# Kernel optimization log

Measured on AMD Instinct MI355X. Metric: run time of the kernel, lower is better.

Reference implementation:

```python
import jax, jax.numpy as jnp
import numpy as np
from jax import lax

B, CIN, H, W = 32, 256, 28, 28
COUT, KS, KEXP = 256, 3, 4
HIDDEN = int(CIN * 0.25)  # ratio hard-coded to 0.25 in the module


def setup_inputs() -> dict:
    key = jax.random.key(0)
    k1, k2, k3, k4 = jax.random.split(key, 4)
    x = jax.random.normal(k1, (B, CIN, H, W), dtype=jnp.float32)
    # SE (InvertedEx) params: fc1 (1x1 conv, no bias), fc2 (1x1 conv, bias)
    fc1_w = jax.random.normal(k2, (HIDDEN, CIN), dtype=jnp.float32) * np.float32(np.sqrt(2.0 / CIN))
    fc2_w = jax.random.normal(k3, (KEXP * COUT, HIDDEN), dtype=jnp.float32) * np.float32(np.sqrt(2.0 / HIDDEN))
    fc2_b = jnp.zeros((KEXP * COUT,), dtype=jnp.float32)
    # K expert conv kernels, he_std = sqrt(2) * (CIN*KS^2)^-0.5
    he_std = np.float32(np.sqrt(2.0) * (CIN * KS * KS) ** -0.5)
    weight = jax.random.normal(k4, (KEXP, COUT, CIN, KS, KS), dtype=jnp.float32) * he_std
    return {"x": x, "fc1_w": fc1_w, "fc2_w": fc2_w, "fc2_b": fc2_b, "weight": weight}


def reference(x, fc1_w, fc2_w, fc2_b, weight):
    # --- SE routing ---
    pooled = jnp.mean(x, axis=(2, 3))                        # [B, CIN]
    h = jax.nn.relu(pooled @ fc1_w.T)                        # [B, HIDDEN]
    y = (h @ fc2_w.T + fc2_b).reshape(B, KEXP, COUT)         # [B, K, COUT]
    prob = jax.nn.softmax(y / jnp.sqrt(jnp.float32(HIDDEN)), axis=1)  # softmax over K
    # --- aggregate per-sample kernels ---
    agg_w = jnp.einsum('bko,koihw->boihw', prob, weight)     # [B, COUT, CIN, KS, KS]
    # --- per-sample conv (batched implicit GEMM via vmap) ---
    def conv1(xi, wi):
        return lax.conv_general_dilated(
            xi[None], wi, window_strides=(1, 1), padding=((1, 1), (1, 1)),
            dimension_numbers=('NCHW', 'OIHW', 'NCHW'))[0]
    out = jax.vmap(conv1)(x, agg_w)                          # [B, COUT, H, W]
    return out
```

## Files before the change

kernel.cpp:

```cpp
#include <hip/hip_runtime.h>
#include <math.h>

#define B_    32
#define CIN_  256
#define HW_   784
#define H_    28
#define W_    28
#define COUT_ 256
#define KEXP_ 4
#define HID_  64

typedef short short8 __attribute__((ext_vector_type(8)));
typedef unsigned short ushort4v __attribute__((ext_vector_type(4)));
typedef float floatx16 __attribute__((ext_vector_type(16)));

__device__ __forceinline__ unsigned short f2bf(float f) {
    union { float f; unsigned int u; } v; v.f = f;
    unsigned int r = (v.u + 0x7FFFu + ((v.u >> 16) & 1u)) >> 16;
    return (unsigned short)r;
}

__global__ __launch_bounds__(256) void xpose_pool_kernel(const float* __restrict__ x,
                                                         unsigned short* __restrict__ x_t,
                                                         float* __restrict__ partial) {
    __shared__ float tile[32][33];
    int bid = blockIdx.x;
    int b   = bid / 200;
    int rem = bid - b * 200;
    int icg = rem / 25;
    int pxt = rem % 25;
    int ic0 = icg * 32;
    int px0 = pxt * 32;
    int t = threadIdx.x;
    int c = t & 31, rr = t >> 5;
    #pragma unroll
    for (int r = 0; r < 4; ++r) {
        int icr = rr + r * 8;
        int px = px0 + c;
        float v = (px < HW_) ? x[((size_t)(b * CIN_ + ic0 + icr)) * HW_ + px] : 0.f;
        tile[icr][c] = v;
    }
    __syncthreads();
    #pragma unroll
    for (int r = 0; r < 4; ++r) {
        int pxr = rr + r * 8;
        int px = px0 + pxr;
        if (px < HW_)
            x_t[((size_t)b * HW_ + px) * CIN_ + ic0 + c] = f2bf(tile[c][pxr]);
    }
    if (t < 32) {
        float s = 0.f;
        #pragma unroll
        for (int cc = 0; cc < 32; ++cc) s += tile[t][cc];
        partial[((size_t)b * 25 + pxt) * CIN_ + ic0 + t] = s * (1.0f / HW_);
    }
}

__global__ __launch_bounds__(256) void pool_kernel(const float* __restrict__ x,
                                                   float* __restrict__ pooled) {
    int w = blockIdx.x * 4 + (threadIdx.x >> 6);
    int lane = threadIdx.x & 63;
    const float* p = x + (size_t)w * HW_;
    float s = 0.f;
    for (int i = lane; i < HW_; i += 64) s += p[i];
    for (int off = 32; off; off >>= 1) s += __shfl_down(s, off);
    if (lane == 0) pooled[w] = s * (1.0f / HW_);
}

__global__ __launch_bounds__(256) void se3_kernel(const float* __restrict__ partial,
                                                  const float* __restrict__ fc1_w,
                                                  const float* __restrict__ fc2_w,
                                                  const float* __restrict__ fc2_b,
                                                  float* __restrict__ prob) {
    __shared__ float pl[CIN_];
    __shared__ float h[HID_];
    __shared__ float wb[16640];
    int b = blockIdx.x, t = threadIdx.x;
    {
        float s = 0.f;
        for (int pt = 0; pt < 25; ++pt)
            s += partial[((size_t)b * 25 + pt) * CIN_ + t];
        pl[t] = s;
    }
    #pragma unroll
    for (int i = 0; i < 16; ++i) {
        int l = t + i * 256;
        float4 v = *(const float4*)(fc1_w + (size_t)l * 4);
        int r = l >> 6, cc = (l & 63) * 4;
        float* dst = &wb[r * 257 + cc];
        dst[0] = v.x; dst[1] = v.y; dst[2] = v.z; dst[3] = v.w;
    }
    __syncthreads();
    if (t < HID_) {
        float s = 0.f;
        const float* wr = &wb[t * 257];
        for (int c = 0; c < CIN_; ++c) s += pl[c] * wr[c];
        h[t] = fmaxf(s, 0.f);
    }
    float yk[KEXP_];
    for (int k = 0; k < KEXP_; ++k) {
        __syncthreads();
        #pragma unroll
        for (int i = 0; i < 16; ++i) {
            int l = t + i * 256;
            float4 v = *(const float4*)(fc2_w + (size_t)k * COUT_ * HID_ + (size_t)l * 4);
            int o = l >> 4, jj = (l & 15) * 4;
            float* dst = &wb[o * 65 + jj];
            dst[0] = v.x; dst[1] = v.y; dst[2] = v.z; dst[3] = v.w;
        }
        __syncthreads();
        float s = fc2_b[k * COUT_ + t];
        const float* wr = &wb[t * 65];
        #pragma unroll
        for (int j = 0; j < HID_; ++j) s += h[j] * wr[j];
        yk[k] = s * 0.125f;
    }
    float m = yk[0];
    for (int k = 1; k < KEXP_; ++k) m = fmaxf(m, yk[k]);
    float e[KEXP_], sum = 0.f;
    for (int k = 0; k < KEXP_; ++k) { e[k] = expf(yk[k] - m); sum += e[k]; }
    float inv = 1.0f / sum;
    for (int k = 0; k < KEXP_; ++k)
        prob[b * (KEXP_ * COUT_) + k * COUT_ + t] = e[k] * inv;
}

__global__ __launch_bounds__(256) void se2_kernel(const float* __restrict__ pooled,
                                                  const float* __restrict__ fc1_w,
                                                  const float* __restrict__ fc2_w,
                                                  const float* __restrict__ fc2_b,
                                                  float* __restrict__ prob) {
    __shared__ float pl[CIN_];
    __shared__ float h[HID_];
    __shared__ float wb[16640];
    int b = blockIdx.x, t = threadIdx.x;
    pl[t] = pooled[b * CIN_ + t];
    #pragma unroll
    for (int i = 0; i < 16; ++i) {
        int l = t + i * 256;
        float4 v = *(const float4*)(fc1_w + (size_t)l * 4);
        int r = l >> 6, cc = (l & 63) * 4;
        float* dst = &wb[r * 257 + cc];
        dst[0] = v.x; dst[1] = v.y; dst[2] = v.z; dst[3] = v.w;
    }
    __syncthreads();
    if (t < HID_) {
        float s = 0.f;
        const float* wr = &wb[t * 257];
        for (int c = 0; c < CIN_; ++c) s += pl[c] * wr[c];
        h[t] = fmaxf(s, 0.f);
    }
    float yk[KEXP_];
    for (int k = 0; k < KEXP_; ++k) {
        __syncthreads();
        #pragma unroll
        for (int i = 0; i < 16; ++i) {
            int l = t + i * 256;
            float4 v = *(const float4*)(fc2_w + (size_t)k * COUT_ * HID_ + (size_t)l * 4);
            int o = l >> 4, jj = (l & 15) * 4;
            float* dst = &wb[o * 65 + jj];
            dst[0] = v.x; dst[1] = v.y; dst[2] = v.z; dst[3] = v.w;
        }
        __syncthreads();
        float s = fc2_b[k * COUT_ + t];
        const float* wr = &wb[t * 65];
        #pragma unroll
        for (int j = 0; j < HID_; ++j) s += h[j] * wr[j];
        yk[k] = s * 0.125f;
    }
    float m = yk[0];
    for (int k = 1; k < KEXP_; ++k) m = fmaxf(m, yk[k]);
    float e[KEXP_], sum = 0.f;
    for (int k = 0; k < KEXP_; ++k) { e[k] = expf(yk[k] - m); sum += e[k]; }
    float inv = 1.0f / sum;
    for (int k = 0; k < KEXP_; ++k)
        prob[b * (KEXP_ * COUT_) + k * COUT_ + t] = e[k] * inv;
}

__global__ __launch_bounds__(256) void agg4_kernel(const float* __restrict__ weight,
                                                   const float* __restrict__ prob,
                                                   unsigned short* __restrict__ agg) {
    __shared__ float ws_w[KEXP_ * CIN_ * 9];
    __shared__ float pb[KEXP_][16];
    int bid = blockIdx.x;
    int oc = bid & 255;
    int b0 = (bid >> 8) * 16;
    int t = threadIdx.x;
    #pragma unroll
    for (int i = 0; i < 9; ++i) {
        int e4 = t + i * 256;
        int k = e4 / 576;
        int r4 = e4 - k * 576;
        float4 v = *(const float4*)(weight + (size_t)k * 589824 + (size_t)oc * 2304 + (size_t)r4 * 4);
        *(float4*)&ws_w[e4 * 4] = v;
    }
    if (t < 64) {
        int k = t >> 4, bb = t & 15;
        pb[k][bb] = prob[(size_t)(b0 + bb) * (KEXP_ * COUT_) + k * COUT_ + oc];
    }
    __syncthreads();
    int icg = t & 63, blane = t >> 6;
    for (int rs = 0; rs < 9; ++rs) {
        float wv[4][4];
        #pragma unroll
        for (int q = 0; q < 4; ++q)
            #pragma unroll
            for (int k = 0; k < 4; ++k)
                wv[q][k] = ws_w[k * 2304 + (icg * 4 + q) * 9 + rs];
        #pragma unroll
        for (int bb = 0; bb < 4; ++bb) {
            int bidx = blane * 4 + bb;
            float p0 = pb[0][bidx], p1 = pb[1][bidx], p2 = pb[2][bidx], p3 = pb[3][bidx];
            ushort4v pack;
            #pragma unroll
            for (int q = 0; q < 4; ++q) {
                float s = p0 * wv[q][0] + p1 * wv[q][1] + p2 * wv[q][2] + p3 * wv[q][3];
                pack[q] = f2bf(s);
            }
            *(ushort4v*)(agg + (((size_t)(b0 + bidx) * 9 + rs) * COUT_ + oc) * CIN_ + icg * 4) = pack;
        }
    }
}

__global__ __launch_bounds__(256, 3) void conv_mfma4_kernel(const unsigned short* __restrict__ x_t,
                                                            const unsigned short* __restrict__ agg,
                                                            float* __restrict__ out) {
    __shared__ __align__(16) short Xs[6 * 35 * 72];

    int gid = blockIdx.x;
    int b      = gid & 31;
    int oc0    = ((gid >> 5) & 1) * 128;
    int rowblk = gid >> 6;
    int py0 = rowblk * 4;

    int t = threadIdx.x;
    int lane = t & 63, w = t >> 6;
    int ml = lane & 31, kh = lane >> 5;

    floatx16 acc[4];
    #pragma unroll
    for (int j = 0; j < 4; ++j)
        #pragma unroll
        for (int r = 0; r < 16; ++r) acc[j][r] = 0.f;

    const unsigned short* xtb = x_t + (size_t)b * HW_ * CIN_;
    const unsigned short* aln = agg + (((size_t)b * 9 * COUT_) + oc0 + w * 32 + ml) * CIN_ + kh * 8;

    short8 Acur0, Acur1, Acur2, Anext0, Anext1, Anext2;
    Acur0 = *(const short8*)(aln + (size_t)0 * (COUT_ * CIN_));
    Acur1 = *(const short8*)(aln + (size_t)3 * (COUT_ * CIN_));
    Acur2 = *(const short8*)(aln + (size_t)6 * (COUT_ * CIN_));
    int dxn = 1, kkn = 0, icn = 0;

    for (int c = 0; c < 4; ++c) {
        if (c) __syncthreads();
        #pragma unroll
        for (int i = 0; i < 7; ++i) {
            int l = t + i * 256;
            if (l < 1680) {
                int pos = l >> 3, g = l & 7;
                int row = pos / 35, col = pos - row * 35;
                int gy = py0 - 1 + row, gx = col - 1;
                short8 v = (short8)0;
                if ((unsigned)gy < 28u && (unsigned)gx < 28u)
                    v = *(const short8*)(xtb + ((size_t)(gy * W_ + gx)) * CIN_ + c * 64 + g * 8);
                *(short8*)&Xs[pos * 72 + g * 8] = v;
            }
        }
        __syncthreads();

        for (int kk = 0; kk < 4; ++kk) {
            for (int dx = 0; dx < 3; ++dx) {
                if (icn < 256) {
                    const unsigned short* ap = aln + icn + kkn * 16;
                    Anext0 = *(const short8*)(ap + (size_t)(0 * 3 + dxn) * (COUT_ * CIN_));
                    Anext1 = *(const short8*)(ap + (size_t)(1 * 3 + dxn) * (COUT_ * CIN_));
                    Anext2 = *(const short8*)(ap + (size_t)(2 * 3 + dxn) * (COUT_ * CIN_));
                    ++dxn;
                    if (dxn == 3) { dxn = 0; ++kkn; if (kkn == 4) { kkn = 0; icn += 64; } }
                }
                int va = (ml + dx) * 72 + kk * 16 + kh * 8;
                #pragma unroll
                for (int r = 0; r < 6; ++r) {
                    short8 Bf = *(const short8*)&Xs[r * 2520 + va];
                    if (r <= 3)
                        acc[r]     = __builtin_amdgcn_mfma_f32_32x32x16_bf16(Acur0, Bf, acc[r], 0, 0, 0);
                    if (r >= 1 && r <= 4)
                        acc[r - 1] = __builtin_amdgcn_mfma_f32_32x32x16_bf16(Acur1, Bf, acc[r - 1], 0, 0, 0);
                    if (r >= 2)
                        acc[r - 2] = __builtin_amdgcn_mfma_f32_32x32x16_bf16(Acur2, Bf, acc[r - 2], 0, 0, 0);
                }
                Acur0 = Anext0; Acur1 = Anext1; Acur2 = Anext2;
            }
        }
    }

    if (ml < W_) {
        #pragma unroll
        for (int j = 0; j < 4; ++j) {
            float* op = out + ((size_t)(b * COUT_ + oc0 + w * 32)) * HW_ + (py0 + j) * W_ + ml;
            #pragma unroll
            for (int r = 0; r < 16; ++r) {
                int ocd = (r & 3) + 8 * (r >> 2) + 4 * kh;
                op[(size_t)ocd * HW_] = acc[j][r];
            }
        }
    }
}

__global__ __launch_bounds__(256) void conv_kernel(const float* __restrict__ x,
                                                   const float* __restrict__ weight,
                                                   const float* __restrict__ prob,
                                                   float* __restrict__ out) {
    __shared__ float xs[30 * 30];
    __shared__ float wagg[8][32][12];
    __shared__ float pl[KEXP_][8];

    int b  = blockIdx.x >> 5;
    int o0 = (blockIdx.x & 31) * 8;
    int t  = threadIdx.x;

    if (t < 32) {
        int k = t >> 3, oc = t & 7;
        pl[k][oc] = prob[b * (KEXP_ * COUT_) + k * COUT_ + o0 + oc];
    }
    int p0 = t;
    int pr[4], pc[4];
    bool pv[4];
    #pragma unroll
    for (int j = 0; j < 4; ++j) {
        int p = p0 + j * 256;
        pv[j] = p < HW_;
        pr[j] = p / W_;
        pc[j] = p % W_;
    }
    float acc[8][4];
    #pragma unroll
    for (int oc = 0; oc < 8; ++oc)
        #pragma unroll
        for (int j = 0; j < 4; ++j) acc[oc][j] = 0.f;

    int aoc = t >> 5, aii = t & 31;

    for (int ic0 = 0; ic0 < CIN_; ic0 += 32) {
        __syncthreads();
        {
            float w9[9];
            #pragma unroll
            for (int j = 0; j < 9; ++j) w9[j] = 0.f;
            int i = ic0 + aii;
            #pragma unroll
            for (int k = 0; k < KEXP_; ++k) {
                float pk = pl[k][aoc];
                const float* wp = weight + ((size_t)(k * COUT_ + o0 + aoc) * CIN_ + i) * 9;
                #pragma unroll
                for (int j = 0; j < 9; ++j) w9[j] += pk * wp[j];
            }
            #pragma unroll
            for (int j = 0; j < 9; ++j) wagg[aoc][aii][j] = w9[j];
        }
        for (int ii = 0; ii < 32; ++ii) {
            int i = ic0 + ii;
            __syncthreads();
            const float* xp = x + (size_t)(b * CIN_ + i) * HW_;
            for (int e = t; e < 900; e += 256) {
                int ry = e / 30, cx = e - ry * 30;
                int gy = ry - 1, gx = cx - 1;
                float v = 0.f;
                if ((unsigned)gy < 28u && (unsigned)gx < 28u) v = xp[gy * W_ + gx];
                xs[e] = v;
            }
            __syncthreads();
            float xv[4][9];
            #pragma unroll
            for (int j = 0; j < 4; ++j) {
                if (pv[j]) {
                    const float* xr = &xs[pr[j] * 30 + pc[j]];
                    xv[j][0] = xr[0];  xv[j][1] = xr[1];  xv[j][2] = xr[2];
                    xv[j][3] = xr[30]; xv[j][4] = xr[31]; xv[j][5] = xr[32];
                    xv[j][6] = xr[60]; xv[j][7] = xr[61]; xv[j][8] = xr[62];
                } else {
                    #pragma unroll
                    for (int q = 0; q < 9; ++q) xv[j][q] = 0.f;
                }
            }
            #pragma unroll
            for (int oc = 0; oc < 8; ++oc) {
                float4 wa = *(const float4*)&wagg[oc][ii][0];
                float4 wb2 = *(const float4*)&wagg[oc][ii][4];
                float  wc = wagg[oc][ii][8];
                #pragma unroll
                for (int j = 0; j < 4; ++j) {
                    acc[oc][j] += xv[j][0] * wa.x + xv[j][1] * wa.y + xv[j][2] * wa.z
                                + xv[j][3] * wa.w + xv[j][4] * wb2.x + xv[j][5] * wb2.y
                                + xv[j][6] * wb2.z + xv[j][7] * wb2.w + xv[j][8] * wc;
                }
            }
        }
    }
    #pragma unroll
    for (int oc = 0; oc < 8; ++oc) {
        float* op = out + (size_t)(b * COUT_ + o0 + oc) * HW_ + p0;
        #pragma unroll
        for (int j = 0; j < 4; ++j)
            if (pv[j]) op[j * 256] = acc[oc][j];
    }
}

extern "C" void kernel_launch(void* const* d_in, const int* in_sizes, int n_in,
                              void* d_out, int out_size, void* d_ws, size_t ws_size,
                              hipStream_t stream) {
    const float* x     = (const float*)d_in[0];
    const float* fc1_w = (const float*)d_in[1];
    const float* fc2_w = (const float*)d_in[2];
    const float* fc2_b = (const float*)d_in[3];
    const float* weight= (const float*)d_in[4];
    float* out = (float*)d_out;

    char* ws = (char*)d_ws;
    float* prob = (float*)(ws);
    unsigned short* x_t = (unsigned short*)(ws + 131072);
    unsigned short* agg = (unsigned short*)(ws + 12976128);
    float* partial = (float*)(ws + 12976128);
    const size_t WS_NEED = 12976128 + (size_t)B_ * 9 * COUT_ * CIN_ * 2;

    if (ws_size >= WS_NEED) {
        xpose_pool_kernel<<<B_ * 8 * 25, 256, 0, stream>>>(x, x_t, partial);
        se3_kernel<<<B_, 256, 0, stream>>>(partial, fc1_w, fc2_w, fc2_b, prob);
        agg4_kernel<<<512, 256, 0, stream>>>(weight, prob, agg);
        conv_mfma4_kernel<<<448, 256, 0, stream>>>(x_t, agg, out);
    } else {
        float* pooled = (float*)(ws + 131072);
        pool_kernel<<<(B_ * CIN_) / 4, 256, 0, stream>>>(x, pooled);
        se2_kernel<<<B_, 256, 0, stream>>>(pooled, fc1_w, fc2_w, fc2_b, prob);
        conv_kernel<<<B_ * (COUT_ / 8), 256, 0, stream>>>(x, weight, prob, out);
    }
}
```

Measured before the change: 158.7 us.

## Fuse fc2+softmax into aggregation kernel and retile MFMA conv to 7-row blocks

The SE kernel is split so that one small kernel computes only the hidden layer. The fc2 projection and the softmax over experts move into the weight-aggregation kernel, which also relayouts the expert weights in shared memory so they can be read as float4 (ic-contiguous per tap). The conv kernel now covers 7 output rows per block with 64 output channels, and splits the waves into two row groups, with 512 blocks and launch bounds of 2. This aims to cut redundant X-tile loads from the 3-row halo and balance the grid, at the cost of more LDS per block and lower occupancy, with uneven work between the 4-row and 3-row wave groups.

```diff
diff --git a/kernel.cpp b/kernel.cpp
--- a/kernel.cpp
+++ b/kernel.cpp
@@ -56,25 +56,11 @@
     }
 }
 
-__global__ __launch_bounds__(256) void pool_kernel(const float* __restrict__ x,
-                                                   float* __restrict__ pooled) {
-    int w = blockIdx.x * 4 + (threadIdx.x >> 6);
-    int lane = threadIdx.x & 63;
-    const float* p = x + (size_t)w * HW_;
-    float s = 0.f;
-    for (int i = lane; i < HW_; i += 64) s += p[i];
-    for (int off = 32; off; off >>= 1) s += __shfl_down(s, off);
-    if (lane == 0) pooled[w] = s * (1.0f / HW_);
-}
-
-__global__ __launch_bounds__(256) void se3_kernel(const float* __restrict__ partial,
-                                                  const float* __restrict__ fc1_w,
-                                                  const float* __restrict__ fc2_w,
-                                                  const float* __restrict__ fc2_b,
-                                                  float* __restrict__ prob) {
+__global__ __launch_bounds__(256) void se_h_kernel(const float* __restrict__ partial,
+                                                   const float* __restrict__ fc1_w,
+                                                   float* __restrict__ h_g) {
     __shared__ float pl[CIN_];
-    __shared__ float h[HID_];
-    __shared__ float wb[16640];
+    __shared__ float wb[64 * 257];
     int b = blockIdx.x, t = threadIdx.x;
     {
         float s = 0.f;
@@ -95,146 +81,104 @@
         float s = 0.f;
         const float* wr = &wb[t * 257];
         for (int c = 0; c < CIN_; ++c) s += pl[c] * wr[c];
-        h[t] = fmaxf(s, 0.f);
-    }
-    float yk[KEXP_];
-    for (int k = 0; k < KEXP_; ++k) {
-        __syncthreads();
-        #pragma unroll
-        for (int i = 0; i < 16; ++i) {
-            int l = t + i * 256;
-            float4 v = *(const float4*)(fc2_w + (size_t)k * COUT_ * HID_ + (size_t)l * 4);
-            int o = l >> 4, jj = (l & 15) * 4;
-            float* dst = &wb[o * 65 + jj];
-            dst[0] = v.x; dst[1] = v.y; dst[2] = v.z; dst[3] = v.w;
-        }
-        __syncthreads();
-        float s = fc2_b[k * COUT_ + t];
-        const float* wr = &wb[t * 65];
-        #pragma unroll
-        for (int j = 0; j < HID_; ++j) s += h[j] * wr[j];
-        yk[k] = s * 0.125f;
-    }
-    float m = yk[0];
-    for (int k = 1; k < KEXP_; ++k) m = fmaxf(m, yk[k]);
-    float e[KEXP_], sum = 0.f;
-    for (int k = 0; k < KEXP_; ++k) { e[k] = expf(yk[k] - m); sum += e[k]; }
-    float inv = 1.0f / sum;
-    for (int k = 0; k < KEXP_; ++k)
-        prob[b * (KEXP_ * COUT_) + k * COUT_ + t] = e[k] * inv;
-}
-
-__global__ __launch_bounds__(256) void se2_kernel(const float* __restrict__ pooled,
-                                                  const float* __restrict__ fc1_w,
-                                                  const float* __restrict__ fc2_w,
-                                                  const float* __restrict__ fc2_b,
-                                                  float* __restrict__ prob) {
-    __shared__ float pl[CIN_];
-    __shared__ float h[HID_];
-    __shared__ float wb[16640];
-    int b = blockIdx.x, t = threadIdx.x;
-    pl[t] = pooled[b * CIN_ + t];
-    #pragma unroll
-    for (int i = 0; i < 16; ++i) {
-        int l = t + i * 256;
-        float4 v = *(const float4*)(fc1_w + (size_t)l * 4);
-        int r = l >> 6, cc = (l & 63) * 4;
-        float* dst = &wb[r * 257 + cc];
-        dst[0] = v.x; dst[1] = v.y; dst[2] = v.z; dst[3] = v.w;
-    }
-    __syncthreads();
-    if (t < HID_) {
-        float s = 0.f;
-        const float* wr = &wb[t * 257];
-        for (int c = 0; c < CIN_; ++c) s += pl[c] * wr[c];
-        h[t] = fmaxf(s, 0.f);
-    }
-    float yk[KEXP_];
-    for (int k = 0; k < KEXP_; ++k) {
-        __syncthreads();
-        #pragma unroll
-        for (int i = 0; i < 16; ++i) {
-            int l = t + i * 256;
-            float4 v = *(const float4*)(fc2_w + (size_t)k * COUT_ * HID_ + (size_t)l * 4);
-            int o = l >> 4, jj = (l & 15) * 4;
-            float* dst = &wb[o * 65 + jj];
-            dst[0] = v.x; dst[1] = v.y; dst[2] = v.z; dst[3] = v.w;
-        }
-        __syncthreads();
-        float s = fc2_b[k * COUT_ + t];
-        const float* wr = &wb[t * 65];
-        #pragma unroll
-        for (int j = 0; j < HID_; ++j) s += h[j] * wr[j];
-        yk[k] = s * 0.125f;
-    }
-    float m = yk[0];
-    for (int k = 1; k < KEXP_; ++k) m = fmaxf(m, yk[k]);
-    float e[KEXP_], sum = 0.f;
-    for (int k = 0; k < KEXP_; ++k) { e[k] = expf(yk[k] - m); sum += e[k]; }
-    float inv = 1.0f / sum;
-    for (int k = 0; k < KEXP_; ++k)
-        prob[b * (KEXP_ * COUT_) + k * COUT_ + t] = e[k] * inv;
-}
-
-__global__ __launch_bounds__(256) void agg4_kernel(const float* __restrict__ weight,
-                                                   const float* __restrict__ prob,
+        h_g[b * HID_ + t] = fmaxf(s, 0.f);
+    }
+}
+
+__global__ __launch_bounds__(256) void agg5_kernel(const float* __restrict__ weight,
+                                                   const float* __restrict__ h_g,
+                                                   const float* __restrict__ fc2_w,
+                                                   const float* __restrict__ fc2_b,
                                                    unsigned short* __restrict__ agg) {
     __shared__ float ws_w[KEXP_ * CIN_ * 9];
-    __shared__ float pb[KEXP_][16];
+    __shared__ float f2s[KEXP_ * HID_];
+    __shared__ float hb[16 * 65];
+    __shared__ float pb[KEXP_ * 16];
     int bid = blockIdx.x;
     int oc = bid & 255;
     int b0 = (bid >> 8) * 16;
     int t = threadIdx.x;
+
     #pragma unroll
     for (int i = 0; i < 9; ++i) {
         int e4 = t + i * 256;
         int k = e4 / 576;
         int r4 = e4 - k * 576;
         float4 v = *(const float4*)(weight + (size_t)k * 589824 + (size_t)oc * 2304 + (size_t)r4 * 4);
-        *(float4*)&ws_w[e4 * 4] = v;
-    }
+        int f = r4 * 4;
+        #pragma unroll
+        for (int q = 0; q < 4; ++q) {
+            int ic = (f + q) / 9, rs = (f + q) - ic * 9;
+            ws_w[k * 2304 + rs * 256 + ic] = ((const float*)&v)[q];
+        }
+    }
+    {
+        int k = t >> 6, j = t & 63;
+        f2s[t] = fc2_w[((size_t)(k * COUT_ + oc)) * HID_ + j];
+    }
+    #pragma unroll
+    for (int i = 0; i < 4; ++i) {
+        int l = t + i * 256;
+        if (l < 16 * HID_) {
+            int bq = l >> 6, j = l & 63;
+            hb[bq * 65 + j] = h_g[(size_t)(b0 + bq) * HID_ + j];
+        }
+    }
+    __syncthreads();
     if (t < 64) {
-        int k = t >> 4, bb = t & 15;
-        pb[k][bb] = prob[(size_t)(b0 + bb) * (KEXP_ * COUT_) + k * COUT_ + oc];
+        int bq = t >> 2, k = t & 3;
+        float s = fc2_b[k * COUT_ + oc];
+        const float* hr = &hb[bq * 65];
+        const float* fr = &f2s[k * HID_];
+        #pragma unroll
+        for (int j = 0; j < HID_; ++j) s += hr[j] * fr[j];
+        float y = s * 0.125f;
+        float m1 = fmaxf(y, __shfl_xor(y, 1));
+        float m  = fmaxf(m1, __shfl_xor(m1, 2));
+        float e = expf(y - m);
+        float s1 = e + __shfl_xor(e, 1);
+        float sm = s1 + __shfl_xor(s1, 2);
+        pb[k * 16 + bq] = e / sm;
     }
     __syncthreads();
+
     int icg = t & 63, blane = t >> 6;
     for (int rs = 0; rs < 9; ++rs) {
-        float wv[4][4];
-        #pragma unroll
-        for (int q = 0; q < 4; ++q)
-            #pragma unroll
-            for (int k = 0; k < 4; ++k)
-                wv[q][k] = ws_w[k * 2304 + (icg * 4 + q) * 9 + rs];
+        float4 w0 = *(const float4*)&ws_w[0 * 2304 + rs * 256 + icg * 4];
+        float4 w1 = *(const float4*)&ws_w[1 * 2304 + rs * 256 + icg * 4];
+        float4 w2 = *(const float4*)&ws_w[2 * 2304 + rs * 256 + icg * 4];
+        float4 w3 = *(const float4*)&ws_w[3 * 2304 + rs * 256 + icg * 4];
         #pragma unroll
         for (int bb = 0; bb < 4; ++bb) {
             int bidx = blane * 4 + bb;
-            float p0 = pb[0][bidx], p1 = pb[1][bidx], p2 = pb[2][bidx], p3 = pb[3][bidx];
+            float p0 = pb[0 * 16 + bidx], p1 = pb[1 * 16 + bidx];
+            float p2 = pb[2 * 16 + bidx], p3 = pb[3 * 16 + bidx];
             ushort4v pack;
-            #pragma unroll
-            for (int q = 0; q < 4; ++q) {
-                float s = p0 * wv[q][0] + p1 * wv[q][1] + p2 * wv[q][2] + p3 * wv[q][3];
-                pack[q] = f2bf(s);
-            }
+            pack[0] = f2bf(p0 * w0.x + p1 * w1.x + p2 * w2.x + p3 * w3.x);
+            pack[1] = f2bf(p0 * w0.y + p1 * w1.y + p2 * w2.y + p3 * w3.y);
+            pack[2] = f2bf(p0 * w0.z + p1 * w1.z + p2 * w2.z + p3 * w3.z);
+            pack[3] = f2bf(p0 * w0.w + p1 * w1.w + p2 * w2.w + p3 * w3.w);
             *(ushort4v*)(agg + (((size_t)(b0 + bidx) * 9 + rs) * COUT_ + oc) * CIN_ + icg * 4) = pack;
         }
     }
 }
 
-__global__ __launch_bounds__(256, 3) void conv_mfma4_kernel(const unsigned short* __restrict__ x_t,
+__global__ __launch_bounds__(256, 2) void conv_mfma5_kernel(const unsigned short* __restrict__ x_t,
                                                             const unsigned short* __restrict__ agg,
                                                             float* __restrict__ out) {
-    __shared__ __align__(16) short Xs[6 * 35 * 72];
+    __shared__ __align__(16) short Xs[9 * 35 * 72];
 
     int gid = blockIdx.x;
     int b      = gid & 31;
-    int oc0    = ((gid >> 5) & 1) * 128;
-    int rowblk = gid >> 6;
-    int py0 = rowblk * 4;
+    int ocq    = (gid >> 5) & 3;
+    int rowblk = gid >> 7;
+    int py0 = rowblk * 7;
 
     int t = threadIdx.x;
     int lane = t & 63, w = t >> 6;
+    int wo = w & 1, wr = w >> 1;
     int ml = lane & 31, kh = lane >> 5;
+    int oc0 = ocq * 64 + wo * 32;
 
     floatx16 acc[4];
     #pragma unroll
@@ -243,7 +187,7 @@
         for (int r = 0; r < 16; ++r) acc[j][r] = 0.f;
 
     const unsigned short* xtb = x_t + (size_t)b * HW_ * CIN_;
-    const unsigned short* aln = agg + (((size_t)b * 9 * COUT_) + oc0 + w * 32 + ml) * CIN_ + kh * 8;
+    const unsigned short* aln = agg + (((size_t)b * 9 * COUT_) + oc0 + ml) * CIN_ + kh * 8;
 
     short8 Acur0, Acur1, Acur2, Anext0, Anext1, Anext2;
     Acur0 = *(const short8*)(aln + (size_t)0 * (COUT_ * CIN_));
@@ -254,9 +198,9 @@
     for (int c = 0; c < 4; ++c) {
         if (c) __syncthreads();
         #pragma unroll
-        for (int i = 0; i < 7; ++i) {
+        for (int i = 0; i < 10; ++i) {
             int l = t + i * 256;
-            if (l < 1680) {
+            if (l < 2520) {
                 int pos = l >> 3, g = l & 7;
                 int row = pos / 35, col = pos - row * 35;
                 int gy = py0 - 1 + row, gx = col - 1;
@@ -279,25 +223,41 @@
                     if (dxn == 3) { dxn = 0; ++kkn; if (kkn == 4) { kkn = 0; icn += 64; } }
                 }
                 int va = (ml + dx) * 72 + kk * 16 + kh * 8;
-                #pragma unroll
-                for (int r = 0; r < 6; ++r) {
-                    short8 Bf = *(const short8*)&Xs[r * 2520 + va];
-                    if (r <= 3)
-                        acc[r]     = __builtin_amdgcn_mfma_f32_32x32x16_bf16(Acur0, Bf, acc[r], 0, 0, 0);
-                    if (r >= 1 && r <= 4)
-                        acc[r - 1] = __builtin_amdgcn_mfma_f32_32x32x16_bf16(Acur1, Bf, acc[r - 1], 0, 0, 0);
-                    if (r >= 2)
-                        acc[r - 2] = __builtin_amdgcn_mfma_f32_32x32x16_bf16(Acur2, Bf, acc[r - 2], 0, 0, 0);
+                if (wr == 0) {
+                    #pragma unroll
+                    for (int r = 0; r < 6; ++r) {
+                        short8 Bf = *(const short8*)&Xs[r * 2520 + va];
+                        if (r <= 3)
+                            acc[r]     = __builtin_amdgcn_mfma_f32_32x32x16_bf16(Acur0, Bf, acc[r], 0, 0, 0);
+                        if (r >= 1 && r <= 4)
+                            acc[r - 1] = __builtin_amdgcn_mfma_f32_32x32x16_bf16(Acur1, Bf, acc[r - 1], 0, 0, 0);
+                        if (r >= 2)
+                            acc[r - 2] = __builtin_amdgcn_mfma_f32_32x32x16_bf16(Acur2, Bf, acc[r - 2], 0, 0, 0);
+                    }
+                } else {
+                    #pragma unroll
+                    for (int rr2 = 0; rr2 < 5; ++rr2) {
+                        int r = rr2 + 4;
+                        short8 Bf = *(const short8*)&Xs[r * 2520 + va];
+                        int j0 = r - 4;
+                        if (j0 <= 2)
+                            acc[j0]     = __builtin_amdgcn_mfma_f32_32x32x16_bf16(Acur0, Bf, acc[j0], 0, 0, 0);
+                        if (r >= 5 && r - 5 <= 2)
+                            acc[r - 5]  = __builtin_amdgcn_mfma_f32_32x32x16_bf16(Acur1, Bf, acc[r - 5], 0, 0, 0);
+                        if (r >= 6)
+                            acc[r - 6]  = __builtin_amdgcn_mfma_f32_32x32x16_bf16(Acur2, Bf, acc[r - 6], 0, 0, 0);
+                    }
                 }
                 Acur0 = Anext0; Acur1 = Anext1; Acur2 = Anext2;
             }
         }
     }
 
+    int jbase = wr * 4;
+    int naccs = wr ? 3 : 4;
     if (ml < W_) {
-        #pragma unroll
-        for (int j = 0; j < 4; ++j) {
-            float* op = out + ((size_t)(b * COUT_ + oc0 + w * 32)) * HW_ + (py0 + j) * W_ + ml;
+        for (int j = 0; j < naccs; ++j) {
+            float* op = out + ((size_t)(b * COUT_ + oc0)) * HW_ + (py0 + jbase + j) * W_ + ml;
             #pragma unroll
             for (int r = 0; r < 16; ++r) {
                 int ocd = (r & 3) + 8 * (r >> 2) + 4 * kh;
@@ -305,6 +265,69 @@
             }
         }
     }
+}
+
+__global__ __launch_bounds__(256) void pool_kernel(const float* __restrict__ x,
+                                                   float* __restrict__ pooled) {
+    int w = blockIdx.x * 4 + (threadIdx.x >> 6);
+    int lane = threadIdx.x & 63;
+    const float* p = x + (size_t)w * HW_;
+    float s = 0.f;
+    for (int i = lane; i < HW_; i += 64) s += p[i];
+    for (int off = 32; off; off >>= 1) s += __shfl_down(s, off);
+    if (lane == 0) pooled[w] = s * (1.0f / HW_);
+}
+
+__global__ __launch_bounds__(256) void se2_kernel(const float* __restrict__ pooled,
+                                                  const float* __restrict__ fc1_w,
+                                                  const float* __restrict__ fc2_w,
+                                                  const float* __restrict__ fc2_b,
+                                                  float* __restrict__ prob) {
+    __shared__ float pl[CIN_];
+    __shared__ float h[HID_];
+    __shared__ float wb[16640];
+    int b = blockIdx.x, t = threadIdx.x;
+    pl[t] = pooled[b * CIN_ + t];
+    #pragma unroll
+    for (int i = 0; i < 16; ++i) {
+        int l = t + i * 256;
+        float4 v = *(const float4*)(fc1_w + (size_t)l * 4);
+        int r = l >> 6, cc = (l & 63) * 4;
+        float* dst = &wb[r * 257 + cc];
+        dst[0] = v.x; dst[1] = v.y; dst[2] = v.z; dst[3] = v.w;
+    }
+    __syncthreads();
+    if (t < HID_) {
+        float s = 0.f;
+        const float* wr = &wb[t * 257];
+        for (int c = 0; c < CIN_; ++c) s += pl[c] * wr[c];
+        h[t] = fmaxf(s, 0.f);
+    }
+    float yk[KEXP_];
+    for (int k = 0; k < KEXP_; ++k) {
+        __syncthreads();
+        #pragma unroll
+        for (int i = 0; i < 16; ++i) {
+            int l = t + i * 256;
+            float4 v = *(const float4*)(fc2_w + (size_t)k * COUT_ * HID_ + (size_t)l * 4);
+            int o = l >> 4, jj = (l & 15) * 4;
+            float* dst = &wb[o * 65 + jj];
+            dst[0] = v.x; dst[1] = v.y; dst[2] = v.z; dst[3] = v.w;
+        }
+        __syncthreads();
+        float s = fc2_b[k * COUT_ + t];
+        const float* wr = &wb[t * 65];
+        #pragma unroll
+        for (int j = 0; j < HID_; ++j) s += h[j] * wr[j];
+        yk[k] = s * 0.125f;
+    }
+    float m = yk[0];
+    for (int k = 1; k < KEXP_; ++k) m = fmaxf(m, yk[k]);
+    float e[KEXP_], sum = 0.f;
+    for (int k = 0; k < KEXP_; ++k) { e[k] = expf(yk[k] - m); sum += e[k]; }
+    float inv = 1.0f / sum;
+    for (int k = 0; k < KEXP_; ++k)
+        prob[b * (KEXP_ * COUT_) + k * COUT_ + t] = e[k] * inv;
 }
 
 __global__ __launch_bounds__(256) void conv_kernel(const float* __restrict__ x,
@@ -417,7 +440,7 @@
     float* out = (float*)d_out;
 
     char* ws = (char*)d_ws;
-    float* prob = (float*)(ws);
+    float* h_g  = (float*)(ws);
     unsigned short* x_t = (unsigned short*)(ws + 131072);
     unsigned short* agg = (unsigned short*)(ws + 12976128);
     float* partial = (float*)(ws + 12976128);
@@ -425,10 +448,11 @@
 
     if (ws_size >= WS_NEED) {
         xpose_pool_kernel<<<B_ * 8 * 25, 256, 0, stream>>>(x, x_t, partial);
-        se3_kernel<<<B_, 256, 0, stream>>>(partial, fc1_w, fc2_w, fc2_b, prob);
-        agg4_kernel<<<512, 256, 0, stream>>>(weight, prob, agg);
-        conv_mfma4_kernel<<<448, 256, 0, stream>>>(x_t, agg, out);
+        se_h_kernel<<<B_, 256, 0, stream>>>(partial, fc1_w, h_g);
+        agg5_kernel<<<512, 256, 0, stream>>>(weight, h_g, fc2_w, fc2_b, agg);
+        conv_mfma5_kernel<<<512, 256, 0, stream>>>(x_t, agg, out);
     } else {
+        float* prob = (float*)(ws);
         float* pooled = (float*)(ws + 131072);
         pool_kernel<<<(B_ * CIN_) / 4, 256, 0, stream>>>(x, pooled);
         se2_kernel<<<B_, 256, 0, stream>>>(pooled, fc1_w, fc2_w, fc2_b, prob);
```

Result: slower. 265.4 us (+67.2%).

## Fuse SE routing into aggregation kernel and widen transpose tile

Applied to the files above, without the earlier changes.

Removes the separate SE kernel: the transpose kernel now handles 64 channels per block with 16-byte bf16 stores and also writes a transposed fc1 weight. The aggregation kernel recomputes pooling, fc1, fc2 and softmax for its 16 samples, which takes one launch and one dependency off the critical path. The cost is redundant SE work in each of the 512 aggregation blocks. The conv kernel's grid and launch bounds change to 512 blocks with an added row guard.

```diff
diff --git a/kernel.cpp b/kernel.cpp
--- a/kernel.cpp
+++ b/kernel.cpp
@@ -20,171 +20,74 @@
     return (unsigned short)r;
 }
 
-__global__ __launch_bounds__(256) void xpose_pool_kernel(const float* __restrict__ x,
-                                                         unsigned short* __restrict__ x_t,
-                                                         float* __restrict__ partial) {
-    __shared__ float tile[32][33];
+__global__ __launch_bounds__(256) void xpose2_kernel(const float* __restrict__ x,
+                                                     const float* __restrict__ fc1_w,
+                                                     unsigned short* __restrict__ x_t,
+                                                     float* __restrict__ partial,
+                                                     float* __restrict__ fc1T) {
+    __shared__ float tile[64][33];
     int bid = blockIdx.x;
-    int b   = bid / 200;
-    int rem = bid - b * 200;
+    int b   = bid / 100;
+    int rem = bid - b * 100;
     int icg = rem / 25;
     int pxt = rem % 25;
-    int ic0 = icg * 32;
+    int ic0 = icg * 64;
     int px0 = pxt * 32;
     int t = threadIdx.x;
-    int c = t & 31, rr = t >> 5;
-    #pragma unroll
-    for (int r = 0; r < 4; ++r) {
-        int icr = rr + r * 8;
-        int px = px0 + c;
+    int pxl = t & 31, icr0 = t >> 5;
+    #pragma unroll
+    for (int r = 0; r < 8; ++r) {
+        int icr = icr0 + r * 8;
+        int px = px0 + pxl;
         float v = (px < HW_) ? x[((size_t)(b * CIN_ + ic0 + icr)) * HW_ + px] : 0.f;
-        tile[icr][c] = v;
+        tile[icr][pxl] = v;
     }
     __syncthreads();
-    #pragma unroll
-    for (int r = 0; r < 4; ++r) {
-        int pxr = rr + r * 8;
-        int px = px0 + pxr;
-        if (px < HW_)
-            x_t[((size_t)b * HW_ + px) * CIN_ + ic0 + c] = f2bf(tile[c][pxr]);
-    }
-    if (t < 32) {
+    if (t < 64) {
         float s = 0.f;
         #pragma unroll
         for (int cc = 0; cc < 32; ++cc) s += tile[t][cc];
         partial[((size_t)b * 25 + pxt) * CIN_ + ic0 + t] = s * (1.0f / HW_);
     }
-}
-
-__global__ __launch_bounds__(256) void pool_kernel(const float* __restrict__ x,
-                                                   float* __restrict__ pooled) {
-    int w = blockIdx.x * 4 + (threadIdx.x >> 6);
-    int lane = threadIdx.x & 63;
-    const float* p = x + (size_t)w * HW_;
-    float s = 0.f;
-    for (int i = lane; i < HW_; i += 64) s += p[i];
-    for (int off = 32; off; off >>= 1) s += __shfl_down(s, off);
-    if (lane == 0) pooled[w] = s * (1.0f / HW_);
-}
-
-__global__ __launch_bounds__(256) void se3_kernel(const float* __restrict__ partial,
-                                                  const float* __restrict__ fc1_w,
-                                                  const float* __restrict__ fc2_w,
-                                                  const float* __restrict__ fc2_b,
-                                                  float* __restrict__ prob) {
-    __shared__ float pl[CIN_];
-    __shared__ float h[HID_];
-    __shared__ float wb[16640];
-    int b = blockIdx.x, t = threadIdx.x;
     {
-        float s = 0.f;
-        for (int pt = 0; pt < 25; ++pt)
-            s += partial[((size_t)b * 25 + pt) * CIN_ + t];
-        pl[t] = s;
-    }
-    #pragma unroll
-    for (int i = 0; i < 16; ++i) {
-        int l = t + i * 256;
-        float4 v = *(const float4*)(fc1_w + (size_t)l * 4);
-        int r = l >> 6, cc = (l & 63) * 4;
-        float* dst = &wb[r * 257 + cc];
-        dst[0] = v.x; dst[1] = v.y; dst[2] = v.z; dst[3] = v.w;
-    }
-    __syncthreads();
-    if (t < HID_) {
-        float s = 0.f;
-        const float* wr = &wb[t * 257];
-        for (int c = 0; c < CIN_; ++c) s += pl[c] * wr[c];
-        h[t] = fmaxf(s, 0.f);
-    }
-    float yk[KEXP_];
-    for (int k = 0; k < KEXP_; ++k) {
-        __syncthreads();
+        int pxl2 = t >> 3, icq = t & 7;
+        int px = px0 + pxl2;
+        if (px < HW_) {
+            unsigned short vals[8];
+            #pragma unroll
+            for (int j = 0; j < 8; ++j) vals[j] = f2bf(tile[icq * 8 + j][pxl2]);
+            *(short8*)(x_t + ((size_t)b * HW_ + px) * CIN_ + ic0 + icq * 8) = *(short8*)vals;
+        }
+    }
+    if (bid == 0) {
         #pragma unroll
         for (int i = 0; i < 16; ++i) {
             int l = t + i * 256;
-            float4 v = *(const float4*)(fc2_w + (size_t)k * COUT_ * HID_ + (size_t)l * 4);
-            int o = l >> 4, jj = (l & 15) * 4;
-            float* dst = &wb[o * 65 + jj];
-            dst[0] = v.x; dst[1] = v.y; dst[2] = v.z; dst[3] = v.w;
-        }
-        __syncthreads();
-        float s = fc2_b[k * COUT_ + t];
-        const float* wr = &wb[t * 65];
-        #pragma unroll
-        for (int j = 0; j < HID_; ++j) s += h[j] * wr[j];
-        yk[k] = s * 0.125f;
-    }
-    float m = yk[0];
-    for (int k = 1; k < KEXP_; ++k) m = fmaxf(m, yk[k]);
-    float e[KEXP_], sum = 0.f;
-    for (int k = 0; k < KEXP_; ++k) { e[k] = expf(yk[k] - m); sum += e[k]; }
-    float inv = 1.0f / sum;
-    for (int k = 0; k < KEXP_; ++k)
-        prob[b * (KEXP_ * COUT_) + k * COUT_ + t] = e[k] * inv;
-}
-
-__global__ __launch_bounds__(256) void se2_kernel(const float* __restrict__ pooled,
-                                                  const float* __restrict__ fc1_w,
-                                                  const float* __restrict__ fc2_w,
-                                                  const float* __restrict__ fc2_b,
-                                                  float* __restrict__ prob) {
-    __shared__ float pl[CIN_];
-    __shared__ float h[HID_];
-    __shared__ float wb[16640];
-    int b = blockIdx.x, t = threadIdx.x;
-    pl[t] = pooled[b * CIN_ + t];
-    #pragma unroll
-    for (int i = 0; i < 16; ++i) {
-        int l = t + i * 256;
-        float4 v = *(const float4*)(fc1_w + (size_t)l * 4);
-        int r = l >> 6, cc = (l & 63) * 4;
-        float* dst = &wb[r * 257 + cc];
-        dst[0] = v.x; dst[1] = v.y; dst[2] = v.z; dst[3] = v.w;
-    }
-    __syncthreads();
-    if (t < HID_) {
-        float s = 0.f;
-        const float* wr = &wb[t * 257];
-        for (int c = 0; c < CIN_; ++c) s += pl[c] * wr[c];
-        h[t] = fmaxf(s, 0.f);
-    }
-    float yk[KEXP_];
-    for (int k = 0; k < KEXP_; ++k) {
-        __syncthreads();
-        #pragma unroll
-        for (int i = 0; i < 16; ++i) {
-            int l = t + i * 256;
-            float4 v = *(const float4*)(fc2_w + (size_t)k * COUT_ * HID_ + (size_t)l * 4);
-            int o = l >> 4, jj = (l & 15) * 4;
-            float* dst = &wb[o * 65 + jj];
-            dst[0] = v.x; dst[1] = v.y; dst[2] = v.z; dst[3] = v.w;
-        }
-        __syncthreads();
-        float s = fc2_b[k * COUT_ + t];
-        const float* wr = &wb[t * 65];
-        #pragma unroll
-        for (int j = 0; j < HID_; ++j) s += h[j] * wr[j];
-        yk[k] = s * 0.125f;
-    }
-    float m = yk[0];
-    for (int k = 1; k < KEXP_; ++k) m = fmaxf(m, yk[k]);
-    float e[KEXP_], sum = 0.f;
-    for (int k = 0; k < KEXP_; ++k) { e[k] = expf(yk[k] - m); sum += e[k]; }
-    float inv = 1.0f / sum;
-    for (int k = 0; k < KEXP_; ++k)
-        prob[b * (KEXP_ * COUT_) + k * COUT_ + t] = e[k] * inv;
-}
-
-__global__ __launch_bounds__(256) void agg4_kernel(const float* __restrict__ weight,
-                                                   const float* __restrict__ prob,
-                                                   unsigned short* __restrict__ agg) {
+            float4 v = *(const float4*)(fc1_w + (size_t)l * 4);
+            int hi = l >> 6, c0 = (l & 63) * 4;
+            fc1T[(size_t)(c0 + 0) * HID_ + hi] = v.x;
+            fc1T[(size_t)(c0 + 1) * HID_ + hi] = v.y;
+            fc1T[(size_t)(c0 + 2) * HID_ + hi] = v.z;
+            fc1T[(size_t)(c0 + 3) * HID_ + hi] = v.w;
+        }
+    }
+}
+
+__global__ __launch_bounds__(256, 2) void agg8_kernel(const float* __restrict__ weight,
+                                                      const float* __restrict__ partial,
+                                                      const float* __restrict__ fc1T,
+                                                      const float* __restrict__ fc2_w,
+                                                      const float* __restrict__ fc2_b,
+                                                      unsigned short* __restrict__ agg) {
     __shared__ float ws_w[KEXP_ * CIN_ * 9];
-    __shared__ float pb[KEXP_][16];
+    __shared__ float pl[16 * 257];
+    __shared__ float hb[16 * 65];
+    __shared__ float pb[KEXP_ * 16];
     int bid = blockIdx.x;
     int oc = bid & 255;
     int b0 = (bid >> 8) * 16;
     int t = threadIdx.x;
+
     #pragma unroll
     for (int i = 0; i < 9; ++i) {
         int e4 = t + i * 256;
@@ -193,9 +96,42 @@
         float4 v = *(const float4*)(weight + (size_t)k * 589824 + (size_t)oc * 2304 + (size_t)r4 * 4);
         *(float4*)&ws_w[e4 * 4] = v;
     }
+    for (int bb = 0; bb < 16; ++bb) {
+        float s = 0.f;
+        for (int pt = 0; pt < 25; ++pt)
+            s += partial[((size_t)(b0 + bb) * 25 + pt) * CIN_ + t];
+        pl[bb * 257 + t] = s;
+    }
+    __syncthreads();
+    {
+        int w = t >> 6, lane = t & 63;
+        float a0 = 0.f, a1 = 0.f, a2 = 0.f, a3 = 0.f;
+        for (int c = 0; c < 256; ++c) {
+            float wv = fc1T[(size_t)c * HID_ + lane];
+            a0 += pl[(w * 4 + 0) * 257 + c] * wv;
+            a1 += pl[(w * 4 + 1) * 257 + c] * wv;
+            a2 += pl[(w * 4 + 2) * 257 + c] * wv;
+            a3 += pl[(w * 4 + 3) * 257 + c] * wv;
+        }
+        hb[(w * 4 + 0) * 65 + lane] = fmaxf(a0, 0.f);
+        hb[(w * 4 + 1) * 65 + lane] = fmaxf(a1, 0.f);
+        hb[(w * 4 + 2) * 65 + lane] = fmaxf(a2, 0.f);
+        hb[(w * 4 + 3) * 65 + lane] = fmaxf(a3, 0.f);
+    }
+    __syncthreads();
     if (t < 64) {
-        int k = t >> 4, bb = t & 15;
-        pb[k][bb] = prob[(size_t)(b0 + bb) * (KEXP_ * COUT_) + k * COUT_ + oc];
+        int bb = t >> 2, k = t & 3;
+        const float* fr = fc2_w + ((size_t)(k * COUT_ + oc)) * HID_;
+        float y = fc2_b[k * COUT_ + oc];
+        #pragma unroll
+        for (int j = 0; j < HID_; ++j) y += hb[bb * 65 + j] * fr[j];
+        y *= 0.125f;
+        float m = fmaxf(y, __shfl_xor(y, 1));
+        m = fmaxf(m, __shfl_xor(m, 2));
+        float e = expf(y - m);
+        float s1 = e + __shfl_xor(e, 1);
+        float s2 = s1 + __shfl_xor(s1, 2);
+        pb[k * 16 + bb] = e / s2;
     }
     __syncthreads();
     int icg = t & 63, blane = t >> 6;
@@ -209,7 +145,8 @@
         #pragma unroll
         for (int bb = 0; bb < 4; ++bb) {
             int bidx = blane * 4 + bb;
-            float p0 = pb[0][bidx], p1 = pb[1][bidx], p2 = pb[2][bidx], p3 = pb[3][bidx];
+            float p0 = pb[0 * 16 + bidx], p1 = pb[1 * 16 + bidx];
+            float p2 = pb[2 * 16 + bidx], p3 = pb[3 * 16 + bidx];
             ushort4v pack;
             #pragma unroll
             for (int q = 0; q < 4; ++q) {
@@ -221,9 +158,9 @@
     }
 }
 
-__global__ __launch_bounds__(256, 3) void conv_mfma4_kernel(const unsigned short* __restrict__ x_t,
-                                                            const unsigned short* __restrict__ agg,
-                                                            float* __restrict__ out) {
+__global__ __launch_bounds__(256, 2) void conv7_kernel(const unsigned short* __restrict__ x_t,
+                                                       const unsigned short* __restrict__ agg,
+                                                       float* __restrict__ out) {
     __shared__ __align__(16) short Xs[6 * 35 * 72];
 
     int gid = blockIdx.x;
@@ -297,14 +234,79 @@
     if (ml < W_) {
         #pragma unroll
         for (int j = 0; j < 4; ++j) {
-            float* op = out + ((size_t)(b * COUT_ + oc0 + w * 32)) * HW_ + (py0 + j) * W_ + ml;
-            #pragma unroll
-            for (int r = 0; r < 16; ++r) {
-                int ocd = (r & 3) + 8 * (r >> 2) + 4 * kh;
-                op[(size_t)ocd * HW_] = acc[j][r];
-            }
-        }
-    }
+            if (py0 + j < H_) {
+                float* op = out + ((size_t)(b * COUT_ + oc0 + w * 32)) * HW_ + (py0 + j) * W_ + ml;
+                #pragma unroll
+                for (int r = 0; r < 16; ++r) {
+                    int ocd = (r & 3) + 8 * (r >> 2) + 4 * kh;
+                    op[(size_t)ocd * HW_] = acc[j][r];
+                }
+            }
+        }
+    }
+}
+
+__global__ __launch_bounds__(256) void pool_kernel(const float* __restrict__ x,
+                                                   float* __restrict__ pooled) {
+    int w = blockIdx.x * 4 + (threadIdx.x >> 6);
+    int lane = threadIdx.x & 63;
+    const float* p = x + (size_t)w * HW_;
+    float s = 0.f;
+    for (int i = lane; i < HW_; i += 64) s += p[i];
+    for (int off = 32; off; off >>= 1) s += __shfl_down(s, off);
+    if (lane == 0) pooled[w] = s * (1.0f / HW_);
+}
+
+__global__ __launch_bounds__(256) void se2_kernel(const float* __restrict__ pooled,
+                                                  const float* __restrict__ fc1_w,
+                                                  const float* __restrict__ fc2_w,
+                                                  const float* __restrict__ fc2_b,
+                                                  float* __restrict__ prob) {
+    __shared__ float pl[CIN_];
+    __shared__ float h[HID_];
+    __shared__ float wb[16640];
+    int b = blockIdx.x, t = threadIdx.x;
+    pl[t] = pooled[b * CIN_ + t];
+    #pragma unroll
+    for (int i = 0; i < 16; ++i) {
+        int l = t + i * 256;
+        float4 v = *(const float4*)(fc1_w + (size_t)l * 4);
+        int r = l >> 6, cc = (l & 63) * 4;
+        float* dst = &wb[r * 257 + cc];
+        dst[0] = v.x; dst[1] = v.y; dst[2] = v.z; dst[3] = v.w;
+    }
+    __syncthreads();
+    if (t < HID_) {
+        float s = 0.f;
+        const float* wr = &wb[t * 257];
+        for (int c = 0; c < CIN_; ++c) s += pl[c] * wr[c];
+        h[t] = fmaxf(s, 0.f);
+    }
+    float yk[KEXP_];
+    for (int k = 0; k < KEXP_; ++k) {
+        __syncthreads();
+        #pragma unroll
+        for (int i = 0; i < 16; ++i) {
+            int l = t + i * 256;
+            float4 v = *(const float4*)(fc2_w + (size_t)k * COUT_ * HID_ + (size_t)l * 4);
+            int o = l >> 4, jj = (l & 15) * 4;
+            float* dst = &wb[o * 65 + jj];
+            dst[0] = v.x; dst[1] = v.y; dst[2] = v.z; dst[3] = v.w;
+        }
+        __syncthreads();
+        float s = fc2_b[k * COUT_ + t];
+        const float* wr = &wb[t * 65];
+        #pragma unroll
+        for (int j = 0; j < HID_; ++j) s += h[j] * wr[j];
+        yk[k] = s * 0.125f;
+    }
+    float m = yk[0];
+    for (int k = 1; k < KEXP_; ++k) m = fmaxf(m, yk[k]);
+    float e[KEXP_], sum = 0.f;
+    for (int k = 0; k < KEXP_; ++k) { e[k] = expf(yk[k] - m); sum += e[k]; }
+    float inv = 1.0f / sum;
+    for (int k = 0; k < KEXP_; ++k)
+        prob[b * (KEXP_ * COUT_) + k * COUT_ + t] = e[k] * inv;
 }
 
 __global__ __launch_bounds__(256) void conv_kernel(const float* __restrict__ x,
@@ -417,18 +419,18 @@
     float* out = (float*)d_out;
 
     char* ws = (char*)d_ws;
-    float* prob = (float*)(ws);
-    unsigned short* x_t = (unsigned short*)(ws + 131072);
-    unsigned short* agg = (unsigned short*)(ws + 12976128);
-    float* partial = (float*)(ws + 12976128);
-    const size_t WS_NEED = 12976128 + (size_t)B_ * 9 * COUT_ * CIN_ * 2;
+    float* partial = (float*)(ws);
+    float* fc1T    = (float*)(ws + 819200);
+    unsigned short* x_t = (unsigned short*)(ws + 884736);
+    unsigned short* agg = (unsigned short*)(ws + 13729792);
+    const size_t WS_NEED = 13729792 + 37748736;
 
     if (ws_size >= WS_NEED) {
-        xpose_pool_kernel<<<B_ * 8 * 25, 256, 0, stream>>>(x, x_t, partial);
-        se3_kernel<<<B_, 256, 0, stream>>>(partial, fc1_w, fc2_w, fc2_b, prob);
-        agg4_kernel<<<512, 256, 0, stream>>>(weight, prob, agg);
-        conv_mfma4_kernel<<<448, 256, 0, stream>>>(x_t, agg, out);
+        xpose2_kernel<<<3200, 256, 0, stream>>>(x, fc1_w, x_t, partial, fc1T);
+        agg8_kernel<<<512, 256, 0, stream>>>(weight, partial, fc1T, fc2_w, fc2_b, agg);
+        conv7_kernel<<<512, 256, 0, stream>>>(x_t, agg, out);
     } else {
+        float* prob = (float*)(ws);
         float* pooled = (float*)(ws + 131072);
         pool_kernel<<<(B_ * CIN_) / 4, 256, 0, stream>>>(x, pooled);
         se2_kernel<<<B_, 256, 0, stream>>>(pooled, fc1_w, fc2_w, fc2_b, prob);
```

Result: slower. 172.5 us (+8.7%).
